# Performance work log

Measured on AMD Instinct MI355X. Metric: run time of the kernel, lower is better.

Reference implementation:

```python
import jax, jax.numpy as jnp
import numpy as np

# ---- architecture constants (from init_kwargs / arch_args) ----
IN_BITS, IN_FRAC, BITS_PER_STREAM = 8, 4, 2
N_STREAMS = IN_BITS // BITS_PER_STREAM          # 4
W_BITS, BITS_PER_SLICE = 8, 2
N_SLICES = W_BITS // BITS_PER_SLICE             # 4
ADC_BITS = 5
ADC_MAX = 2.0 ** ADC_BITS - 1.0                 # 31
SUBARRAY_SIZE = 128
IC, OC, K, STRIDE, PAD = 64, 64, 3, 1, 1
F_TOTAL = IC * K * K                            # 576 unfolded features
N_SUB = (F_TOTAL + SUBARRAY_SIZE - 1) // SUBARRAY_SIZE  # 5 subarrays
CHUNK = -(-F_TOTAL // N_SUB)                    # 116, matches torch.chunk sizes


def bit_stream(x):
    """VectorizedInputBitStreaming.forward: fixed-point quantize + two's complement + bit-serial split."""
    int_bits = IN_BITS - IN_FRAC - 1
    max_val = 2.0 ** int_bits - 2.0 ** (-IN_FRAC)
    q = jnp.round(jnp.clip(x, -(2.0 ** int_bits), max_val) * (2 ** IN_FRAC)).astype(jnp.int32)
    q = jnp.where(q < 0, (1 << IN_BITS) + q, q)  # two's complement encode
    shifts = jnp.arange(0, IN_BITS, BITS_PER_STREAM, dtype=jnp.int32)
    return ((q[..., None] >> shifts) & ((1 << BITS_PER_STREAM) - 1)).astype(jnp.float32)


def bit_slice(w):
    """VectorizedWeightBitSlicing.forward: pos/neg split, normalize by max abs, integer bit-slice."""
    wp = jnp.maximum(w, 0.0)
    wn = jnp.maximum(-w, 0.0)
    max_abs = jnp.maximum(wp.max(), wn.max())
    max_abs = jnp.where(max_abs > 0, max_abs, 1.0)
    mv = 2 ** W_BITS - 1
    pi = jnp.round(wp / max_abs * mv).astype(jnp.int32)
    ni = jnp.round(wn / max_abs * mv).astype(jnp.int32)
    shifts = jnp.arange(0, W_BITS, BITS_PER_SLICE, dtype=jnp.int32)
    mask = (1 << BITS_PER_SLICE) - 1
    pos = ((pi[..., None] >> shifts) & mask).astype(jnp.float32)
    neg = ((ni[..., None] >> shifts) & mask).astype(jnp.float32)
    return pos, neg, max_abs


def adc(x):
    """Nbit_ADC simulated: uniform round + clip to [0, 2^adc_bits - 1]."""
    return jnp.clip(jnp.round(x), 0.0, ADC_MAX)


def _forward(inputs, weight):
    # unfold -> (B, IC*K*K, H', W') with (c, kh, kw)-major feature ordering like F.unfold
    patches = jax.lax.conv_general_dilated_patches(
        inputs, (K, K), (STRIDE, STRIDE), [(PAD, PAD), (PAD, PAD)])
    B, F, H, W = patches.shape
    P = H * W
    patches = patches.reshape(B, F, P)

    streams = bit_stream(patches)                     # (B, F, P, S)
    pos_sl, neg_sl, norm = bit_slice(weight)
    pos_m = pos_sl.reshape(OC, F, N_SLICES)           # (O, F, T)
    neg_m = neg_sl.reshape(OC, F, N_SLICES)

    # zero-pad feature dim to N_SUB*CHUNK and reshape into subarray chunks
    pad = N_SUB * CHUNK - F
    streams = jnp.pad(streams, ((0, 0), (0, pad), (0, 0), (0, 0))).reshape(B, N_SUB, CHUNK, P, N_STREAMS)
    pos_m = jnp.pad(pos_m, ((0, 0), (0, pad), (0, 0))).reshape(OC, N_SUB, CHUNK, N_SLICES)
    neg_m = jnp.pad(neg_m, ((0, 0), (0, pad), (0, 0))).reshape(OC, N_SUB, CHUNK, N_SLICES)

    # per-subarray analog MAC: (c, b, o, p, s, t)
    pos_r = jnp.einsum('bcfps,ocft->cbopst', streams, pos_m)
    neg_r = jnp.einsum('bcfps,ocft->cbopst', streams, neg_m)

    # ADC quantize, then weight by 2^(stream*bits) * 2^(slice*bits), sum over s,t and subarrays c
    scale = (2.0 ** (jnp.arange(N_STREAMS) * BITS_PER_STREAM))[:, None] * \
            (2.0 ** (jnp.arange(N_SLICES) * BITS_PER_SLICE))[None, :]
    diff = jnp.einsum('cbopst,st->bop', adc(pos_r) - adc(neg_r), scale)

    out = diff * norm / (2.0 ** IN_BITS - 1.0)
    return out.reshape(B, OC, H, W), jnp.float32(0.0)


def setup_inputs() -> dict:
    key = jax.random.key(0)
    k1, k2 = jax.random.split(key)
    inputs = jax.random.normal(k1, (4, IC, 32, 32), dtype=jnp.float32)
    # kaiming_normal_-like init
    weight = jax.random.normal(k2, (OC, IC, K, K), dtype=jnp.float32) * (2.0 / (IC * K * K)) ** 0.5
    return {"inputs": inputs, "weight": weight}


def reference(inputs, weight):
    return _forward(inputs, weight)
```

## Files before the change

### kernel.cpp

```cpp
#include <hip/hip_runtime.h>
#include <stdint.h>


typedef int v4i __attribute__((ext_vector_type(4)));
typedef unsigned int v4u __attribute__((ext_vector_type(4)));

#define WS_NORM   0
#define WS_B      1024
#define WS_AQ     331776
#define B_PLANE   40960

__device__ __forceinline__ unsigned char quant_in(float x) {
  x = fminf(fmaxf(x, -8.0f), 7.9375f);
  int q = (int)rintf(x * 16.0f);
  return (unsigned char)(q & 255);
}

__global__ __launch_bounds__(256) void k_prep(
    const float* __restrict__ in, const float* __restrict__ w,
    unsigned char* __restrict__ Aq, unsigned char* __restrict__ Bq,
    float* __restrict__ nrm, float* __restrict__ out_scalar)
{
  __shared__ float smax[4];
  int bid = blockIdx.x, tid = threadIdx.x;
  if (bid < 2560) {
    if (bid == 0 && tid == 0) out_scalar[0] = 0.0f;
    unsigned int widx = bid * 256 + tid;
    unsigned int m  = ((widx >> 5) * 52429u) >> 18;
    unsigned int kw = widx - m * 160;
    int b = m >> 10, p = m & 1023;
    int y = p >> 5, x = p & 31;
    unsigned int pack = 0;
    #pragma unroll
    for (int i = 0; i < 4; ++i) {
      unsigned int k = kw * 4 + i;
      unsigned int c = k >> 7;
      unsigned int j = k & 127;
      unsigned int csize = (c == 4) ? 112 : 116;
      unsigned int bv = 0;
      if (j < csize) {
        unsigned int f  = c * 116 + j;
        unsigned int ic = (f * 7282u) >> 16;
        unsigned int r9 = f - ic * 9;
        unsigned int dy = (r9 * 11u) >> 5;
        unsigned int dx = r9 - dy * 3;
        int iy = y + (int)dy - 1, ix = x + (int)dx - 1;
        if (iy >= 0 && iy < 32 && ix >= 0 && ix < 32)
          bv = quant_in(in[((b * 64 + ic) * 32 + iy) * 32 + ix]);
      }
      pack |= bv << (8 * i);
    }
    ((unsigned int*)Aq)[widx] = pack;
  } else {
    int q = bid - 2560;
    float a = 0.0f;
    #pragma unroll 4
    for (int i = 0; i < 36; ++i) {
      float4 v = ((const float4*)w)[i * 256 + tid];
      a = fmaxf(a, fmaxf(fmaxf(fabsf(v.x), fabsf(v.y)),
                         fmaxf(fabsf(v.z), fabsf(v.w))));
    }
    #pragma unroll
    for (int off = 32; off > 0; off >>= 1)
      a = fmaxf(a, __shfl_down(a, off, 64));
    if ((tid & 63) == 0) smax[tid >> 6] = a;
    __syncthreads();
    float norm = fmaxf(fmaxf(smax[0], smax[1]), fmaxf(smax[2], smax[3]));
    norm = (norm > 0.0f) ? norm : 1.0f;
    if (q == 0 && tid == 0) nrm[0] = norm;
    float sc = 255.0f / norm;

    unsigned int* Bd = (unsigned int*)Bq;
    for (int g = 0; g < 9; ++g) {
      int grp = g * 1024 + q * 256 + tid;
      unsigned int m4 = (unsigned)grp >> 4;
      unsigned int oc = (m4 * 7282u) >> 16;
      unsigned int fg = (unsigned)grp - oc * 144;
      unsigned int f  = fg * 4;
      unsigned int c  = (f * 565u) >> 16;
      unsigned int j  = f - c * 116;
      unsigned int col = c * 32 + (j >> 2);
      float4 wv = ((const float4*)w)[grp];
      int p0 = (int)rintf(fmaxf(wv.x, 0.0f) * sc);
      int p1 = (int)rintf(fmaxf(wv.y, 0.0f) * sc);
      int p2 = (int)rintf(fmaxf(wv.z, 0.0f) * sc);
      int p3 = (int)rintf(fmaxf(wv.w, 0.0f) * sc);
      int n0 = (int)rintf(fmaxf(-wv.x, 0.0f) * sc);
      int n1 = (int)rintf(fmaxf(-wv.y, 0.0f) * sc);
      int n2 = (int)rintf(fmaxf(-wv.z, 0.0f) * sc);
      int n3 = (int)rintf(fmaxf(-wv.w, 0.0f) * sc);
      unsigned int Pp = (unsigned)p0 | ((unsigned)p1 << 8) |
                        ((unsigned)p2 << 16) | ((unsigned)p3 << 24);
      unsigned int Pn = (unsigned)n0 | ((unsigned)n1 << 8) |
                        ((unsigned)n2 << 16) | ((unsigned)n3 << 24);
      #pragma unroll
      for (int t = 0; t < 4; ++t) {
        Bd[((t)     * 64 + oc) * 160 + col] = (Pp >> (2 * t)) & 0x03030303u;
        Bd[((4 + t) * 64 + oc) * 160 + col] = (Pn >> (2 * t)) & 0x03030303u;
      }
    }
    int gtid = q * 256 + tid;
    #pragma unroll
    for (int e = 0; e < 8; ++e) {
      int idx = gtid * 8 + e;
      int plane = idx >> 10;
      int r = idx & 1023;
      int oc = r >> 4;
      int s = r & 15;
      int c, d;
      if (s < 12) { c = (s * 11) >> 5; d = 29 + s - 3 * c; }
      else        { c = 4;             d = s + 16; }
      Bd[(plane * 64 + oc) * 160 + c * 32 + d] = 0u;
    }
  }
}

__device__ __forceinline__ v4i bits2(v4u w, int s) {
  v4u r = (w >> (unsigned)(2 * s)) & 0x03030303u;
  return (v4i)r;
}

__global__ __launch_bounds__(256) void k_main(
    const unsigned char* __restrict__ Aq, const unsigned char* __restrict__ Bq,
    const float* __restrict__ nrm, float* __restrict__ out)
{
  int tid   = threadIdx.x;
  int lane  = tid & 63;
  int wave  = tid >> 6;
  int mtile = blockIdx.x >> 2;
  int otile = blockIdx.x & 3;

  int r16  = lane & 15;
  int kgrp = lane >> 4;
  int m = mtile * 64 + wave * 16 + r16;
  const unsigned char* ap = Aq + m * 640 + kgrp * 16;
  const unsigned char* bp = Bq + (otile * 16 + r16) * 640 + kgrp * 16;
  float fsc = nrm[0] / 255.0f;

  v4i outacc = {0, 0, 0, 0};

  #pragma unroll
  for (int c = 0; c < 5; ++c) {
    v4u a0 = *(const v4u*)(ap + c * 128);
    v4u a1 = *(const v4u*)(ap + c * 128 + 64);
    v4i b0[8], b1[8];
    #pragma unroll
    for (int pl = 0; pl < 8; ++pl) {
      b0[pl] = *(const v4i*)(bp + pl * B_PLANE + c * 128);
      b1[pl] = *(const v4i*)(bp + pl * B_PLANE + c * 128 + 64);
    }

    #pragma unroll
    for (int s = 0; s < 4; ++s) {
      v4i as0 = bits2(a0, s), as1 = bits2(a1, s);
      #pragma unroll
      for (int t = 0; t < 4; ++t) {
        v4i z = {0, 0, 0, 0};
        v4i pacc = __builtin_amdgcn_mfma_i32_16x16x64_i8(as0, b0[t], z, 0, 0, 0);
        pacc     = __builtin_amdgcn_mfma_i32_16x16x64_i8(as1, b1[t], pacc, 0, 0, 0);
        v4i nacc = __builtin_amdgcn_mfma_i32_16x16x64_i8(as0, b0[4 + t], z, 0, 0, 0);
        nacc     = __builtin_amdgcn_mfma_i32_16x16x64_i8(as1, b1[4 + t], nacc, 0, 0, 0);
        int sh = 2 * (s + t);
        #pragma unroll
        for (int r = 0; r < 4; ++r) {
          int d = (pacc[r] < 31 ? pacc[r] : 31) - (nacc[r] < 31 ? nacc[r] : 31);
          outacc[r] += d << sh;
        }
      }
    }
  }

  int oc = otile * 16 + r16;
  #pragma unroll
  for (int r = 0; r < 4; ++r) {
    int mo = mtile * 64 + wave * 16 + kgrp * 4 + r;
    int b = mo >> 10, p = mo & 1023;
    out[(b * 64 + oc) * 1024 + p] = (float)outacc[r] * fsc;
  }
}

extern "C" void kernel_launch(void* const* d_in, const int* in_sizes, int n_in,
                              void* d_out, int out_size, void* d_ws, size_t ws_size,
                              hipStream_t stream) {
  const float* inp = (const float*)d_in[0];
  const float* wgt = (const float*)d_in[1];
  float* out = (float*)d_out;
  unsigned char* ws = (unsigned char*)d_ws;

  float*         nrm = (float*)(ws + WS_NORM);
  unsigned char* Bq  = ws + WS_B;
  unsigned char* Aq  = ws + WS_AQ;

  k_prep<<<2564, 256, 0, stream>>>(inp, wgt, Aq, Bq, nrm, out + 262144);
  k_main<<<256, 256, 0, stream>>>(Aq, Bq, nrm, out);
}
```

Before: 88.96 us.

## Store packed 8-bit weights once and stage per-otile slice in swizzled LDS

Weights are now stored as full 8-bit packed values, split into positive and negative groups with an XOR swizzle, instead of eight pre-sliced 2-bit planes. This cuts the B footprint fourfold. Each k_main block copies its 20KB output-tile slice into shared memory and extracts the 2-bit slices in registers. The aim is less global traffic and fewer register-held B loads, at the cost of 20KB of LDS per block, a barrier, and extra shift/mask ALU work. The prep grid grows to 2569 blocks, so the weight path uses 9 blocks.

Result: faster. 82.15 us (-7.7%).

```diff
diff --git a/kernel.cpp b/kernel.cpp
--- a/kernel.cpp
+++ b/kernel.cpp
@@ -7,8 +7,9 @@
 
 #define WS_NORM   0
 #define WS_B      1024
-#define WS_AQ     331776
-#define B_PLANE   40960
+#define WS_AQ     131072
+#define B_SLICE   20480
+#define B_SG      10240
 
 __device__ __forceinline__ unsigned char quant_in(float x) {
   x = fminf(fmaxf(x, -8.0f), 7.9375f);
@@ -18,7 +19,7 @@
 
 __global__ __launch_bounds__(256) void k_prep(
     const float* __restrict__ in, const float* __restrict__ w,
-    unsigned char* __restrict__ Aq, unsigned char* __restrict__ Bq,
+    unsigned char* __restrict__ Aq, unsigned char* __restrict__ Bqb,
     float* __restrict__ nrm, float* __restrict__ out_scalar)
 {
   __shared__ float smax[4];
@@ -70,16 +71,16 @@
     if (q == 0 && tid == 0) nrm[0] = norm;
     float sc = 255.0f / norm;
 
-    unsigned int* Bd = (unsigned int*)Bq;
-    for (int g = 0; g < 9; ++g) {
-      int grp = g * 1024 + q * 256 + tid;
-      unsigned int m4 = (unsigned)grp >> 4;
-      unsigned int oc = (m4 * 7282u) >> 16;
-      unsigned int fg = (unsigned)grp - oc * 144;
-      unsigned int f  = fg * 4;
-      unsigned int c  = (f * 565u) >> 16;
-      unsigned int j  = f - c * 116;
-      unsigned int col = c * 32 + (j >> 2);
+    #pragma unroll
+    for (int g = 0; g < 4; ++g) {
+      int grp = (q * 4 + g) * 256 + tid;
+      unsigned int gf = (unsigned)grp * 4u;
+      unsigned int oc = gf / 576u;
+      unsigned int f  = gf - oc * 576u;
+      unsigned int c  = f / 116u;
+      unsigned int j  = f - c * 116u;
+      unsigned int base = (oc >> 4) * B_SLICE + (oc & 15) * 640 + c * 128 + j;
+      unsigned int key  = (oc & 7) << 4;
       float4 wv = ((const float4*)w)[grp];
       int p0 = (int)rintf(fmaxf(wv.x, 0.0f) * sc);
       int p1 = (int)rintf(fmaxf(wv.y, 0.0f) * sc);
@@ -93,24 +94,22 @@
                         ((unsigned)p2 << 16) | ((unsigned)p3 << 24);
       unsigned int Pn = (unsigned)n0 | ((unsigned)n1 << 8) |
                         ((unsigned)n2 << 16) | ((unsigned)n3 << 24);
-      #pragma unroll
-      for (int t = 0; t < 4; ++t) {
-        Bd[((t)     * 64 + oc) * 160 + col] = (Pp >> (2 * t)) & 0x03030303u;
-        Bd[((4 + t) * 64 + oc) * 160 + col] = (Pn >> (2 * t)) & 0x03030303u;
-      }
-    }
-    int gtid = q * 256 + tid;
-    #pragma unroll
-    for (int e = 0; e < 8; ++e) {
-      int idx = gtid * 8 + e;
-      int plane = idx >> 10;
-      int r = idx & 1023;
-      int oc = r >> 4;
-      int s = r & 15;
+      *(unsigned int*)(Bqb + (base ^ key))          = Pp;
+      *(unsigned int*)(Bqb + ((base + B_SG) ^ key)) = Pn;
+    }
+
+    int tg = q * 256 + tid;
+    if (tg < 2048) {
+      int slice = tg >> 9;
+      int r  = tg & 511;
+      int sg = r >> 8;
+      int rr = r & 255;
+      int row = rr >> 4, s = rr & 15;
       int c, d;
-      if (s < 12) { c = (s * 11) >> 5; d = 29 + s - 3 * c; }
-      else        { c = 4;             d = s + 16; }
-      Bd[(plane * 64 + oc) * 160 + c * 32 + d] = 0u;
+      if (s < 12) { c = s / 3; d = 29 + s - 3 * c; }
+      else        { c = 4;     d = 16 + s; }
+      unsigned int base = slice * B_SLICE + sg * B_SG + row * 640 + c * 128 + d * 4;
+      *(unsigned int*)(Bqb + (base ^ (((unsigned)row & 7) << 4))) = 0u;
     }
   }
 }
@@ -121,20 +120,30 @@
 }
 
 __global__ __launch_bounds__(256) void k_main(
-    const unsigned char* __restrict__ Aq, const unsigned char* __restrict__ Bq,
+    const unsigned char* __restrict__ Aq, const unsigned char* __restrict__ Bqb,
     const float* __restrict__ nrm, float* __restrict__ out)
 {
+  __shared__ __align__(16) unsigned char Bl[B_SLICE];
+
   int tid   = threadIdx.x;
   int lane  = tid & 63;
   int wave  = tid >> 6;
   int mtile = blockIdx.x >> 2;
   int otile = blockIdx.x & 3;
 
+  const unsigned char* src = Bqb + otile * B_SLICE;
+  #pragma unroll
+  for (int i = 0; i < 5; ++i)
+    *(v4u*)(Bl + i * 4096 + tid * 16) = *(const v4u*)(src + i * 4096 + tid * 16);
+  __syncthreads();
+
   int r16  = lane & 15;
   int kgrp = lane >> 4;
   int m = mtile * 64 + wave * 16 + r16;
   const unsigned char* ap = Aq + m * 640 + kgrp * 16;
-  const unsigned char* bp = Bq + (otile * 16 + r16) * 640 + kgrp * 16;
+  unsigned int key = ((unsigned)r16 & 7) << 4;
+  unsigned int b0o = ((unsigned)(r16 * 640 + kgrp * 16)) ^ key;
+  unsigned int b1o = ((unsigned)(r16 * 640 + kgrp * 16 + 64)) ^ key;
   float fsc = nrm[0] / 255.0f;
 
   v4i outacc = {0, 0, 0, 0};
@@ -143,11 +152,16 @@
   for (int c = 0; c < 5; ++c) {
     v4u a0 = *(const v4u*)(ap + c * 128);
     v4u a1 = *(const v4u*)(ap + c * 128 + 64);
-    v4i b0[8], b1[8];
-    #pragma unroll
-    for (int pl = 0; pl < 8; ++pl) {
-      b0[pl] = *(const v4i*)(bp + pl * B_PLANE + c * 128);
-      b1[pl] = *(const v4i*)(bp + pl * B_PLANE + c * 128 + 64);
+    v4u p0 = *(const v4u*)(Bl + b0o + c * 128);
+    v4u p1 = *(const v4u*)(Bl + b1o + c * 128);
+    v4u n0 = *(const v4u*)(Bl + b0o + B_SG + c * 128);
+    v4u n1 = *(const v4u*)(Bl + b1o + B_SG + c * 128);
+
+    v4i btp0[4], btp1[4], btn0[4], btn1[4];
+    #pragma unroll
+    for (int t = 0; t < 4; ++t) {
+      btp0[t] = bits2(p0, t); btp1[t] = bits2(p1, t);
+      btn0[t] = bits2(n0, t); btn1[t] = bits2(n1, t);
     }
 
     #pragma unroll
@@ -156,10 +170,10 @@
       #pragma unroll
       for (int t = 0; t < 4; ++t) {
         v4i z = {0, 0, 0, 0};
-        v4i pacc = __builtin_amdgcn_mfma_i32_16x16x64_i8(as0, b0[t], z, 0, 0, 0);
-        pacc     = __builtin_amdgcn_mfma_i32_16x16x64_i8(as1, b1[t], pacc, 0, 0, 0);
-        v4i nacc = __builtin_amdgcn_mfma_i32_16x16x64_i8(as0, b0[4 + t], z, 0, 0, 0);
-        nacc     = __builtin_amdgcn_mfma_i32_16x16x64_i8(as1, b1[4 + t], nacc, 0, 0, 0);
+        v4i pacc = __builtin_amdgcn_mfma_i32_16x16x64_i8(as0, btp0[t], z, 0, 0, 0);
+        pacc     = __builtin_amdgcn_mfma_i32_16x16x64_i8(as1, btp1[t], pacc, 0, 0, 0);
+        v4i nacc = __builtin_amdgcn_mfma_i32_16x16x64_i8(as0, btn0[t], z, 0, 0, 0);
+        nacc     = __builtin_amdgcn_mfma_i32_16x16x64_i8(as1, btn1[t], nacc, 0, 0, 0);
         int sh = 2 * (s + t);
         #pragma unroll
         for (int r = 0; r < 4; ++r) {
@@ -188,9 +202,9 @@
   unsigned char* ws = (unsigned char*)d_ws;
 
   float*         nrm = (float*)(ws + WS_NORM);
-  unsigned char* Bq  = ws + WS_B;
+  unsigned char* Bqb = ws + WS_B;
   unsigned char* Aq  = ws + WS_AQ;
 
-  k_prep<<<2564, 256, 0, stream>>>(inp, wgt, Aq, Bq, nrm, out + 262144);
-  k_main<<<256, 256, 0, stream>>>(Aq, Bq, nrm, out);
-}
+  k_prep<<<2569, 256, 0, stream>>>(inp, wgt, Aq, Bqb, nrm, out + 262144);
+  k_main<<<256, 256, 0, stream>>>(Aq, Bqb, nrm, out);
+}
```
